# Kernel tuning notes

Hardware: AMD Instinct MI355X
Metric: run time of the kernel (lower is better)

Reference implementation:

```python
import jax, jax.numpy as jnp
import numpy as np

B, S, D = 1, 4096, 1024
H, DH = 8, 128
SCALING = 256.0 ** -0.5
SOFTCAP = 50.0
WINDOW = 512
EPS = 1e-6
NEG = -1e30


def setup_inputs() -> dict:
    key = jax.random.key(0)
    ks = jax.random.split(key, 8)
    hidden_states = jax.random.normal(ks[0], (B, S, D), dtype=jnp.float32)
    # rope tables: plausible cos/sin in [-1,1]
    inv_freq = 1.0 / (10000.0 ** (jnp.arange(0, DH, 2, dtype=jnp.float32) / DH))
    t = jnp.arange(S, dtype=jnp.float32)
    freqs = jnp.outer(t, inv_freq)  # [S, DH/2]
    emb = jnp.concatenate([freqs, freqs], axis=-1)  # [S, DH]
    cos = jnp.cos(emb)[None]  # [1, S, DH]
    sin = jnp.sin(emb)[None]
    w = 0.02
    Wq = jax.random.normal(ks[1], (H * DH, D), dtype=jnp.float32) * w
    Wk = jax.random.normal(ks[2], (H * DH, D), dtype=jnp.float32) * w
    Wv = jax.random.normal(ks[3], (H * DH, D), dtype=jnp.float32) * w
    Wo = jax.random.normal(ks[4], (D, H * DH), dtype=jnp.float32) * w
    q_norm_w = jnp.zeros((DH,), dtype=jnp.float32)
    k_norm_w = jnp.zeros((DH,), dtype=jnp.float32)
    return {"hidden_states": hidden_states, "cos": cos, "sin": sin,
            "Wq": Wq, "Wk": Wk, "Wv": Wv, "Wo": Wo,
            "q_norm_w": q_norm_w, "k_norm_w": k_norm_w}


def _rms_norm(x, w):
    # Gemma3 RMSNorm: x * rsqrt(mean(x^2) + eps) * (1 + w)
    var = jnp.mean(jnp.square(x), axis=-1, keepdims=True)
    return x * jax.lax.rsqrt(var + EPS) * (1.0 + w)


def _rotate_half(x):
    x1, x2 = jnp.split(x, 2, axis=-1)
    return jnp.concatenate([-x2, x1], axis=-1)


def reference(hidden_states, cos, sin, Wq, Wk, Wv, Wo, q_norm_w, k_norm_w):
    b, s, _ = hidden_states.shape
    # QKV projections -> [B, H, S, DH]
    q = (hidden_states @ Wq.T).reshape(b, s, H, DH).transpose(0, 2, 1, 3)
    k = (hidden_states @ Wk.T).reshape(b, s, H, DH).transpose(0, 2, 1, 3)
    v = (hidden_states @ Wv.T).reshape(b, s, H, DH).transpose(0, 2, 1, 3)
    # per-head RMSNorm on q and k
    q = _rms_norm(q, q_norm_w)
    k = _rms_norm(k, k_norm_w)
    # RoPE (cos/sin broadcast over heads via unsqueeze(1))
    c = cos[:, None, :, :]
    si = sin[:, None, :, :]
    q = q * c + _rotate_half(q) * si
    k = k * c + _rotate_half(k) * si
    # scores with scaling and logit softcapping
    scores = jnp.einsum('bhqd,bhkd->bhqk', q, k) * SCALING
    scores = SOFTCAP * jnp.tanh(scores / SOFTCAP)
    # causal + sliding-window mask: attend to j with 0 <= i - j < WINDOW (plus j == i)
    i = jnp.arange(s)[:, None]
    j = jnp.arange(s)[None, :]
    mask = (j <= i) & (i - j < WINDOW)  # [S, S]
    scores = jnp.where(mask[None, None], scores, NEG)
    probs = jax.nn.softmax(scores, axis=-1)  # [B, H, S, S]
    attn = jnp.einsum('bhqk,bhkd->bhqd', probs, v)
    attn = attn.transpose(0, 2, 1, 3).reshape(b, s, H * DH)
    out = attn @ Wo.T
    return out, probs
```

## Files before the change

### kernel.cpp

```cpp
#include <hip/hip_runtime.h>

#define S_LEN 4096

typedef _Float16 f16;
typedef __bf16 bf16;
typedef __attribute__((ext_vector_type(4))) _Float16 f16x4;
typedef __attribute__((ext_vector_type(8))) _Float16 f16x8;
typedef __attribute__((ext_vector_type(8))) __bf16 bf16x8;
typedef __attribute__((ext_vector_type(4))) float f32x4;

__device__ __forceinline__ void async_cp16(void* lds, const void* g) {
  __builtin_amdgcn_global_load_lds((const __attribute__((address_space(1))) void*)g,
                                   (__attribute__((address_space(3))) void*)lds, 16, 0, 0);
}

__device__ __forceinline__ f32x4 mfma16(f16x8 a, f16x8 b, f32x4 c) {
  return __builtin_amdgcn_mfma_f32_16x16x32_f16(a, b, c, 0, 0, 0);
}

__global__ void detect_dtype(const unsigned short* __restrict__ x, int* __restrict__ flag) {
  const int t = threadIdx.x;
  int cnt = 0;
  for (int i = t; i < 16384; i += 256) {
    const int e = (x[i] >> 7) & 0xFF;
    cnt += (e >= 0x87);
  }
#pragma unroll
  for (int m = 1; m < 64; m <<= 1) cnt += __shfl_xor(cnt, m);
  __shared__ int red[4];
  if ((t & 63) == 0) red[t >> 6] = cnt;
  __syncthreads();
  if (t == 0) *flag = (red[0] + red[1] + red[2] + red[3] > 64) ? 1 : 0;
}

__device__ __forceinline__ void cvt8(const void* src, f16* dst, int i, int fp) {
  f16x8 o;
  if (fp) {
    const float* s = (const float*)src;
#pragma unroll
    for (int j = 0; j < 8; ++j) o[j] = (f16)s[i + j];
  } else {
    const bf16x8 v = *(const bf16x8*)((const bf16*)src + i);
#pragma unroll
    for (int j = 0; j < 8; ++j) o[j] = (f16)(float)v[j];
  }
  *(f16x8*)(dst + i) = o;
}

__global__ void cvt_all(const void* __restrict__ hs, const void* __restrict__ wq,
                        const void* __restrict__ wk, const void* __restrict__ wv,
                        const void* __restrict__ wo, const void* __restrict__ c,
                        const void* __restrict__ s, const void* __restrict__ qn,
                        const void* __restrict__ kn, f16* __restrict__ hsf,
                        f16* __restrict__ wqkv, f16* __restrict__ woh,
                        float* __restrict__ cd, float* __restrict__ sd,
                        float* __restrict__ qnd, float* __restrict__ knd,
                        const int* __restrict__ flagp) {
  const int fp = *flagp;
  const int b = blockIdx.x, tid = threadIdx.x;
  if (b < 2048) {
    cvt8(hs, hsf, (b * 256 + tid) * 8, fp);
  } else if (b < 4096) {
    const int bb = b - 2048;
    const int sub = bb >> 9;
    const int i = ((bb & 511) * 256 + tid) * 8;
    const void* src = (sub == 0) ? wq : (sub == 1) ? wk : (sub == 2) ? wv : wo;
    f16* dst = (sub < 3) ? (wqkv + (size_t)sub * 1048576) : woh;
    cvt8(src, dst, i, fp);
  } else if (b < 8192) {
    const int bb = b - 4096;
    const void* src = (bb < 2048) ? c : s;
    float* dst = (bb < 2048) ? cd : sd;
    const int i = (bb & 2047) * 256 + tid;
    dst[i] = fp ? ((const float*)src)[i] : (float)((const bf16*)src)[i];
  } else {
    if (tid < 128) qnd[tid] = fp ? ((const float*)qn)[tid] : (float)((const bf16*)qn)[tid];
    else knd[tid - 128] = fp ? ((const float*)kn)[tid - 128] : (float)((const bf16*)kn)[tid - 128];
  }
}

__launch_bounds__(256, 2)
__global__ void gemm_qkv(const f16* __restrict__ A, const f16* __restrict__ B,
                         const float* __restrict__ cosp, const float* __restrict__ sinp,
                         const float* __restrict__ qnw, const float* __restrict__ knw,
                         f16* __restrict__ qh, f16* __restrict__ kh, f16* __restrict__ vt) {
  __shared__ f16 smem[16384];
  f16* As = smem;
  f16* Bs = smem + 8192;
  const int tid = threadIdx.x;
  const int w = tid >> 6, l = tid & 63;
  const int n0 = blockIdx.x * 128, m0 = blockIdx.y * 128;
  const int wm = (w >> 1) * 64, wn = (w & 1) * 64;
  f32x4 acc[4][4] = {};
  for (int k0 = 0; k0 < 1024; k0 += 64) {
#pragma unroll
    for (int it = 0; it < 4; ++it) {
      const int c = it * 4 + w;
      const int row = c * 8 + (l >> 3);
      const int dq = (l & 7) ^ (row & 7);
      async_cp16(&As[c * 512], &A[(size_t)(m0 + row) * 1024 + k0 + dq * 8]);
      async_cp16(&Bs[c * 512], &B[(size_t)(n0 + row) * 1024 + k0 + dq * 8]);
    }
    __syncthreads();
#pragma unroll
    for (int ks = 0; ks < 2; ++ks) {
      f16x8 af[4], bfr[4];
#pragma unroll
      for (int i = 0; i < 4; ++i) {
        const int ra = wm + i * 16 + (l & 15);
        af[i] = *(const f16x8*)&As[ra * 64 + (((ks * 4 + (l >> 4)) ^ (ra & 7)) << 3)];
        const int rb = wn + i * 16 + (l & 15);
        bfr[i] = *(const f16x8*)&Bs[rb * 64 + (((ks * 4 + (l >> 4)) ^ (rb & 7)) << 3)];
      }
#pragma unroll
      for (int mi = 0; mi < 4; ++mi)
#pragma unroll
        for (int ni = 0; ni < 4; ++ni)
          acc[mi][ni] = mfma16(af[mi], bfr[ni], acc[mi][ni]);
    }
    __syncthreads();
  }
  const int part = blockIdx.x >> 3;
  const int h = blockIdx.x & 7;
#pragma unroll
  for (int mi = 0; mi < 4; ++mi)
#pragma unroll
    for (int ni = 0; ni < 4; ++ni) {
      const int col = wn + ni * 16 + (l & 15);
#pragma unroll
      for (int r = 0; r < 4; ++r) {
        const int row = wm + mi * 16 + ((l >> 4) << 2) + r;
        smem[row * 128 + (col ^ (((row >> 3) & 7) << 3))] = (f16)acc[mi][ni][r];
      }
    }
  __syncthreads();
  if (part == 2) {
#pragma unroll
    for (int it = 0; it < 8; ++it) {
      const int idx = it * 256 + tid;
      const int dh = idx >> 4;
      const int sl = (idx & 15) * 8;
      f16x8 o;
#pragma unroll
      for (int k = 0; k < 8; ++k)
        o[k] = smem[(sl + k) * 128 + (dh ^ ((((sl + k) >> 3) & 7) << 3))];
      *(f16x8*)&vt[((size_t)(h * 128 + dh)) * S_LEN + m0 + sl] = o;
    }
  } else {
    const float* nw = part ? knw : qnw;
    f16* outb = part ? kh : qh;
    const float nw0 = 1.f + nw[l], nw1 = 1.f + nw[l + 64];
#pragma unroll 4
    for (int rr = 0; rr < 32; ++rr) {
      const int row = w * 32 + rr;
      const int sg = m0 + row;
      const int cs = ((row >> 3) & 7) << 3;
      const float x0 = (float)smem[row * 128 + (l ^ cs)];
      const float x1 = (float)smem[row * 128 + ((l + 64) ^ cs)];
      float ssum = x0 * x0 + x1 * x1;
#pragma unroll
      for (int m = 1; m < 64; m <<= 1) ssum += __shfl_xor(ssum, m);
      const float rn = rsqrtf(ssum * (1.f / 128.f) + 1e-6f);
      const float g0 = rn * nw0, g1 = rn * nw1;
      const float c0 = cosp[sg * 128 + l], c1 = cosp[sg * 128 + l + 64];
      const float s0 = sinp[sg * 128 + l], s1 = sinp[sg * 128 + l + 64];
      f16* o = outb + ((size_t)h * S_LEN + sg) * 128;
      o[l] = (f16)(x0 * g0 * c0 - x1 * g1 * s0);
      o[l + 64] = (f16)(x1 * g1 * c1 + x0 * g0 * s1);
    }
  }
}

__launch_bounds__(256, 2)
__global__ void attn64(const f16* __restrict__ Qh, const f16* __restrict__ Kh,
                       const f16* __restrict__ Vt, f16* __restrict__ Pc,
                       float* __restrict__ Lsg, f16* __restrict__ Oh) {
  __shared__ f16 Qs[64 * 128];
  __shared__ f16 Ks[2 * 64 * 128];
  __shared__ f16 Vs[2 * 128 * 64];
  const int tid = threadIdx.x, w = tid >> 6, l = tid & 63;
  const int q0 = blockIdx.x * 64, h = blockIdx.y;
  const int kt0 = (q0 >= 512) ? ((q0 - 511) >> 6) : 0;
  const int kt1 = (q0 + 64) >> 6;

#pragma unroll
  for (int it = 0; it < 4; ++it) {
    const int c = it * 4 + w;
    const int row = c * 4 + (l >> 4);
    const int dq = (l & 15) ^ (row & 15);
    async_cp16(&Qs[c * 512], &Qh[((size_t)h * S_LEN + q0 + row) * 128 + dq * 8]);
  }
#pragma unroll
  for (int it = 0; it < 4; ++it) {
    const int c = it * 4 + w;
    { const int row = c * 4 + (l >> 4);
      const int dq = (l & 15) ^ (row & 15);
      async_cp16(&Ks[c * 512], &Kh[((size_t)h * S_LEN + kt0 * 64 + row) * 128 + dq * 8]); }
    { const int row = c * 8 + (l >> 3);
      const int dq = (l & 7) ^ (row & 7);
      async_cp16(&Vs[c * 512], &Vt[((size_t)h * 128 + row) * S_LEN + kt0 * 64 + dq * 8]); }
  }
  __syncthreads();
  f16x8 qfrag[4];
#pragma unroll
  for (int ks = 0; ks < 4; ++ks) {
    const int r = w * 16 + (l & 15);
    qfrag[ks] = *(const f16x8*)&Qs[r * 128 + (((ks * 4 + (l >> 4)) ^ (r & 15)) << 3)];
  }
  __syncthreads();

  f16* Ps = Qs + w * 1024;
  float l_i[4] = {0.f, 0.f, 0.f, 0.f};
  f32x4 oacc[8] = {};

  for (int t = kt0; t < kt1; ++t) {
    const int cur = (t - kt0) & 1;
    const int kb = cur * 8192, vb = cur * 8192;
    if (t + 1 < kt1) {
      const int nb = (cur ^ 1) * 8192;
#pragma unroll
      for (int it = 0; it < 4; ++it) {
        const int c = it * 4 + w;
        { const int row = c * 4 + (l >> 4);
          const int dq = (l & 15) ^ (row & 15);
          async_cp16(&Ks[nb + c * 512],
                     &Kh[((size_t)h * S_LEN + (t + 1) * 64 + row) * 128 + dq * 8]); }
        { const int row = c * 8 + (l >> 3);
          const int dq = (l & 7) ^ (row & 7);
          async_cp16(&Vs[nb + c * 512],
                     &Vt[((size_t)h * 128 + row) * S_LEN + (t + 1) * 64 + dq * 8]); }
      }
    }
    f32x4 sacc[4] = {};
    __builtin_amdgcn_s_setprio(1);
#pragma unroll
    for (int ks = 0; ks < 4; ++ks) {
      f16x8 kfrag[4];
#pragma unroll
      for (int ni = 0; ni < 4; ++ni) {
        const int r = ni * 16 + (l & 15);
        kfrag[ni] = *(const f16x8*)&Ks[kb + r * 128 + (((ks * 4 + (l >> 4)) ^ (r & 15)) << 3)];
      }
#pragma unroll
      for (int ni = 0; ni < 4; ++ni)
        sacc[ni] = mfma16(qfrag[ks], kfrag[ni], sacc[ni]);
    }
    __builtin_amdgcn_s_setprio(0);
#pragma unroll
    for (int reg = 0; reg < 4; ++reg) {
      const int pr = ((l >> 4) << 2) + reg;
      const int q = q0 + w * 16 + pr;
      float rs = 0.f;
#pragma unroll
      for (int ni = 0; ni < 4; ++ni) {
        const int col = t * 64 + ni * 16 + (l & 15);
        float s = sacc[ni][reg] * 0.0625f;
        const float z = __expf(s * 0.04f);
        s = 50.f * (1.f - 2.f / (z + 1.f));
        const bool valid = (col <= q) && (q - col < 512);
        const float p = valid ? __expf(s - 8.f) : 0.f;
        rs += p;
        const int pc = ni * 16 + (l & 15);
        Ps[pr * 64 + (((pc >> 3) ^ (pr & 7)) << 3) + (pc & 7)] = (f16)p;
      }
#pragma unroll
      for (int m = 1; m < 16; m <<= 1) rs += __shfl_xor(rs, m);
      l_i[reg] += rs;
    }
    __builtin_amdgcn_s_setprio(1);
#pragma unroll
    for (int ks = 0; ks < 2; ++ks) {
      const int rp = l & 15;
      const f16x8 pf = *(const f16x8*)&Ps[rp * 64 + (((ks * 4 + (l >> 4)) ^ (rp & 7)) << 3)];
      f16x8 vf[8];
#pragma unroll
      for (int ni = 0; ni < 8; ++ni) {
        const int r = ni * 16 + (l & 15);
        vf[ni] = *(const f16x8*)&Vs[vb + r * 64 + (((ks * 4 + (l >> 4)) ^ (r & 7)) << 3)];
      }
#pragma unroll
      for (int ni = 0; ni < 8; ++ni)
        oacc[ni] = mfma16(pf, vf[ni], oacc[ni]);
    }
    __builtin_amdgcn_s_setprio(0);
    {
      const size_t rowbase = (size_t)h * 4096 + q0 + w * 16;
#pragma unroll
      for (int i = 0; i < 4; ++i) {
        const int pr = i * 4 + (l >> 4);
        const int pc = (l & 15) * 4;
        const f16x4 v = *(const f16x4*)&Ps[pr * 64 + (((pc >> 3) ^ (pr & 7)) << 3) + (pc & 7)];
        *(f16x4*)&Pc[(rowbase + pr) * 576 + (t - kt0) * 64 + pc] = v;
      }
    }
    __syncthreads();
  }

  float il[4];
#pragma unroll
  for (int r = 0; r < 4; ++r) il[r] = 1.f / l_i[r];
  if ((l & 15) == 0) {
#pragma unroll
    for (int r = 0; r < 4; ++r)
      Lsg[(h << 12) + q0 + w * 16 + ((l >> 4) << 2) + r] = il[r];
  }
#pragma unroll
  for (int ni = 0; ni < 8; ++ni) {
    const int row = q0 + w * 16 + ((l >> 4) << 2);
    const int col = h * 128 + ni * 16 + (l & 15);
#pragma unroll
    for (int r = 0; r < 4; ++r)
      Oh[(size_t)(row + r) * 1024 + col] = (f16)(oacc[ni][r] * il[r]);
  }
}

__launch_bounds__(256, 2)
__global__ void gemmO_probs(const f16* __restrict__ A, const f16* __restrict__ B,
                            void* __restrict__ dout, const f16* __restrict__ Pc,
                            const float* __restrict__ Lsg, const int* __restrict__ flagp) {
  __shared__ f16 smem[16384];
  const int fp = *flagp;
  const int tid = threadIdx.x;
  if (blockIdx.x < 256) {
    f16* As = smem;
    f16* Bs = smem + 8192;
    const int w = tid >> 6, l = tid & 63;
    const int n0 = (blockIdx.x & 7) * 128, m0 = (blockIdx.x >> 3) * 128;
    const int wm = (w >> 1) * 64, wn = (w & 1) * 64;
    f32x4 acc[4][4] = {};
    for (int k0 = 0; k0 < 1024; k0 += 64) {
#pragma unroll
      for (int it = 0; it < 4; ++it) {
        const int c = it * 4 + w;
        const int row = c * 8 + (l >> 3);
        const int dq = (l & 7) ^ (row & 7);
        async_cp16(&As[c * 512], &A[(size_t)(m0 + row) * 1024 + k0 + dq * 8]);
        async_cp16(&Bs[c * 512], &B[(size_t)(n0 + row) * 1024 + k0 + dq * 8]);
      }
      __syncthreads();
#pragma unroll
      for (int ks = 0; ks < 2; ++ks) {
        f16x8 af[4], bfr[4];
#pragma unroll
        for (int i = 0; i < 4; ++i) {
          const int ra = wm + i * 16 + (l & 15);
          af[i] = *(const f16x8*)&As[ra * 64 + (((ks * 4 + (l >> 4)) ^ (ra & 7)) << 3)];
          const int rb = wn + i * 16 + (l & 15);
          bfr[i] = *(const f16x8*)&Bs[rb * 64 + (((ks * 4 + (l >> 4)) ^ (rb & 7)) << 3)];
        }
#pragma unroll
        for (int mi = 0; mi < 4; ++mi)
#pragma unroll
          for (int ni = 0; ni < 4; ++ni)
            acc[mi][ni] = mfma16(af[mi], bfr[ni], acc[mi][ni]);
      }
      __syncthreads();
    }
#pragma unroll
    for (int mi = 0; mi < 4; ++mi)
#pragma unroll
      for (int ni = 0; ni < 4; ++ni) {
        const int col = n0 + wn + ni * 16 + (l & 15);
        const int row = m0 + wm + mi * 16 + ((l >> 4) << 2);
#pragma unroll
        for (int r = 0; r < 4; ++r) {
          const size_t off = (size_t)(row + r) * 1024 + col;
          if (fp) ((float*)dout)[off] = acc[mi][ni][r];
          else    ((bf16*)dout)[off] = (bf16)acc[mi][ni][r];
        }
      }
  } else {
    const long long stride = (long long)(gridDim.x - 256) * 256;
    const long long base = (long long)(blockIdx.x - 256) * 256 + tid;
    if (fp) {
      float* pb = (float*)dout + 4194304;
      const long long total = 8LL * 4096 * 1024;
      auto do4 = [&](long long idx) {
        const int h = (int)(idx >> 22);
        const int rem = (int)(idx & 4194303);
        const int row = rem >> 10;
        const int c = (rem & 1023) << 2;
        const int q0r = row & ~63;
        const int jc0 = (q0r >= 512) ? (((q0r - 511) >> 6) << 6) : 0;
        f32x4 v = {};
        if (c >= jc0 && c < q0r + 64) {
          const float sc = Lsg[(h << 12) + row];
          const f16x4 pv = *(const f16x4*)&Pc[((size_t)(h << 12) + row) * 576 + (c - jc0)];
#pragma unroll
          for (int k = 0; k < 4; ++k) v[k] = (float)pv[k] * sc;
        }
        __builtin_nontemporal_store(v, (f32x4*)&pb[((size_t)h << 24) + ((size_t)row << 12) + c]);
      };
      for (long long i0 = base; i0 < total; i0 += 2 * stride) {
        do4(i0);
        if (i0 + stride < total) do4(i0 + stride);
      }
    } else {
      bf16* pb = (bf16*)dout + 4194304;
      const long long total = 8LL * 4096 * 512;
      auto do8 = [&](long long idx) {
        const int h = (int)(idx >> 21);
        const int rem = (int)(idx & 2097151);
        const int row = rem >> 9;
        const int c = (rem & 511) << 3;
        const int q0r = row & ~63;
        const int jc0 = (q0r >= 512) ? (((q0r - 511) >> 6) << 6) : 0;
        bf16x8 v = {};
        if (c >= jc0 && c < q0r + 64) {
          const float sc = Lsg[(h << 12) + row];
          const f16x8 pv = *(const f16x8*)&Pc[((size_t)(h << 12) + row) * 576 + (c - jc0)];
#pragma unroll
          for (int k = 0; k < 8; ++k) v[k] = (bf16)((float)pv[k] * sc);
        }
        __builtin_nontemporal_store(v, (bf16x8*)&pb[((size_t)h << 24) + ((size_t)row << 12) + c]);
      };
      for (long long i0 = base; i0 < total; i0 += 2 * stride) {
        do8(i0);
        if (i0 + stride < total) do8(i0 + stride);
      }
    }
  }
}

extern "C" void kernel_launch(void* const* d_in, const int* in_sizes, int n_in,
                              void* d_out, int out_size, void* d_ws, size_t ws_size,
                              hipStream_t stream) {
  (void)in_sizes; (void)n_in; (void)out_size; (void)ws_size;
  char* ws = (char*)d_ws;
  f16*   Pc    = (f16*)(ws);
  f16*   qh    = (f16*)(ws + (36u << 20));
  f16*   kh    = (f16*)(ws + (44u << 20));
  f16*   vt    = (f16*)(ws + (52u << 20));
  f16*   attnh = (f16*)(ws + (60u << 20));
  f16*   woh   = (f16*)(ws + (68u << 20));
  f16*   hsf   = (f16*)(ws + (70u << 20));
  float* Lsg   = (float*)(ws + (70u << 20));
  f16*   wqkv  = (f16*)(ws + (78u << 20));
  float* cosf  = (float*)(ws + (84u << 20));
  float* sinf  = (float*)(ws + (86u << 20));
  float* qnwf  = (float*)(ws + (88u << 20));
  float* knwf  = (float*)(ws + (88u << 20) + 512);
  int*   flag  = (int*)(ws + (88u << 20) + 1024);

  detect_dtype<<<1, 256, 0, stream>>>((const unsigned short*)d_in[0], flag);
  cvt_all<<<8193, 256, 0, stream>>>(d_in[0], d_in[3], d_in[4], d_in[5], d_in[6],
                                    d_in[1], d_in[2], d_in[7], d_in[8],
                                    hsf, wqkv, woh, cosf, sinf, qnwf, knwf, flag);
  gemm_qkv<<<dim3(24, 32), 256, 0, stream>>>(hsf, wqkv, cosf, sinf, qnwf, knwf, qh, kh, vt);
  attn64<<<dim3(64, 8), 256, 0, stream>>>(qh, kh, vt, Pc, Lsg, attnh);
  gemmO_probs<<<2048, 256, 0, stream>>>(attnh, woh, d_out, Pc, Lsg, flag);
}
```

Before: 670.1 us.

## Move probs zero-fill into QKV GEMM launch and write only the band later

After: 676.7 us. No clear change (+1.0%).

```diff
diff --git a/kernel.cpp b/kernel.cpp
--- a/kernel.cpp
+++ b/kernel.cpp
@@ -79,17 +79,56 @@
   }
 }
 
+__device__ __forceinline__ void probs_zero_fill(void* dout, int fp, int fb, int nfb) {
+  const int tid = threadIdx.x;
+  if (fp) {
+    float* pb = (float*)dout + 4194304;
+    const int total = 8 * 4096 * 880;
+    const f32x4 z = {};
+    for (int u = fb * 256 + tid; u < total; u += nfb * 256) {
+      const int rowid = (int)((unsigned)u / 880u);
+      const int cu = u - rowid * 880;
+      const int row = rowid & 4095;
+      const int q0r = row & ~63;
+      const int jc0 = (q0r >= 512) ? (((q0r - 511) >> 6) << 6) : 0;
+      const int jc0c = jc0 >> 2;
+      const int c4 = (cu < jc0c) ? (cu << 2) : (jc0 + 576 + ((cu - jc0c) << 2));
+      __builtin_nontemporal_store(z, (f32x4*)&pb[((size_t)rowid << 12) + c4]);
+    }
+  } else {
+    bf16* pb = (bf16*)dout + 4194304;
+    const int total = 8 * 4096 * 440;
+    const bf16x8 z = {};
+    for (int u = fb * 256 + tid; u < total; u += nfb * 256) {
+      const int rowid = (int)((unsigned)u / 440u);
+      const int cu = u - rowid * 440;
+      const int row = rowid & 4095;
+      const int q0r = row & ~63;
+      const int jc0 = (q0r >= 512) ? (((q0r - 511) >> 6) << 6) : 0;
+      const int jc0c = jc0 >> 3;
+      const int c8 = (cu < jc0c) ? (cu << 3) : (jc0 + 576 + ((cu - jc0c) << 3));
+      __builtin_nontemporal_store(z, (bf16x8*)&pb[((size_t)rowid << 12) + c8]);
+    }
+  }
+}
+
 __launch_bounds__(256, 2)
 __global__ void gemm_qkv(const f16* __restrict__ A, const f16* __restrict__ B,
                          const float* __restrict__ cosp, const float* __restrict__ sinp,
                          const float* __restrict__ qnw, const float* __restrict__ knw,
-                         f16* __restrict__ qh, f16* __restrict__ kh, f16* __restrict__ vt) {
+                         f16* __restrict__ qh, f16* __restrict__ kh, f16* __restrict__ vt,
+                         void* __restrict__ dout, const int* __restrict__ flagp) {
   __shared__ f16 smem[16384];
+  const int id = blockIdx.x;
+  if (id >= 768) {
+    probs_zero_fill(dout, *flagp, id - 768, gridDim.x - 768);
+    return;
+  }
   f16* As = smem;
   f16* Bs = smem + 8192;
   const int tid = threadIdx.x;
   const int w = tid >> 6, l = tid & 63;
-  const int n0 = blockIdx.x * 128, m0 = blockIdx.y * 128;
+  const int n0 = (id % 24) * 128, m0 = (id / 24) * 128;
   const int wm = (w >> 1) * 64, wn = (w & 1) * 64;
   f32x4 acc[4][4] = {};
   for (int k0 = 0; k0 < 1024; k0 += 64) {
@@ -120,8 +159,8 @@
     }
     __syncthreads();
   }
-  const int part = blockIdx.x >> 3;
-  const int h = blockIdx.x & 7;
+  const int part = (id % 24) >> 3;
+  const int h = id & 7;
 #pragma unroll
   for (int mi = 0; mi < 4; ++mi)
 #pragma unroll
@@ -370,53 +409,44 @@
         }
       }
   } else {
-    const long long stride = (long long)(gridDim.x - 256) * 256;
-    const long long base = (long long)(blockIdx.x - 256) * 256 + tid;
+    const int bb = blockIdx.x - 256, nbb = gridDim.x - 256;
     if (fp) {
       float* pb = (float*)dout + 4194304;
-      const long long total = 8LL * 4096 * 1024;
-      auto do4 = [&](long long idx) {
-        const int h = (int)(idx >> 22);
-        const int rem = (int)(idx & 4194303);
-        const int row = rem >> 10;
-        const int c = (rem & 1023) << 2;
+      const int total = 8 * 4096 * 144;
+      for (int u = bb * 256 + tid; u < total; u += nbb * 256) {
+        const int rowid = (int)((unsigned)u / 144u);
+        const int cu = u - rowid * 144;
+        const int row = rowid & 4095;
         const int q0r = row & ~63;
         const int jc0 = (q0r >= 512) ? (((q0r - 511) >> 6) << 6) : 0;
+        const int c4 = jc0 + (cu << 2);
         f32x4 v = {};
-        if (c >= jc0 && c < q0r + 64) {
-          const float sc = Lsg[(h << 12) + row];
-          const f16x4 pv = *(const f16x4*)&Pc[((size_t)(h << 12) + row) * 576 + (c - jc0)];
+        if (c4 < q0r + 64) {
+          const float sc = Lsg[rowid];
+          const f16x4 pv = *(const f16x4*)&Pc[(size_t)rowid * 576 + (cu << 2)];
 #pragma unroll
           for (int k = 0; k < 4; ++k) v[k] = (float)pv[k] * sc;
         }
-        __builtin_nontemporal_store(v, (f32x4*)&pb[((size_t)h << 24) + ((size_t)row << 12) + c]);
-      };
-      for (long long i0 = base; i0 < total; i0 += 2 * stride) {
-        do4(i0);
-        if (i0 + stride < total) do4(i0 + stride);
+        __builtin_nontemporal_store(v, (f32x4*)&pb[((size_t)rowid << 12) + c4]);
       }
     } else {
       bf16* pb = (bf16*)dout + 4194304;
-      const long long total = 8LL * 4096 * 512;
-      auto do8 = [&](long long idx) {
-        const int h = (int)(idx >> 21);
-        const int rem = (int)(idx & 2097151);
-        const int row = rem >> 9;
-        const int c = (rem & 511) << 3;
+      const int total = 8 * 4096 * 72;
+      for (int u = bb * 256 + tid; u < total; u += nbb * 256) {
+        const int rowid = (int)((unsigned)u / 72u);
+        const int cu = u - rowid * 72;
+        const int row = rowid & 4095;
         const int q0r = row & ~63;
         const int jc0 = (q0r >= 512) ? (((q0r - 511) >> 6) << 6) : 0;
+        const int c8 = jc0 + (cu << 3);
         bf16x8 v = {};
-        if (c >= jc0 && c < q0r + 64) {
-          const float sc = Lsg[(h << 12) + row];
-          const f16x8 pv = *(const f16x8*)&Pc[((size_t)(h << 12) + row) * 576 + (c - jc0)];
+        if (c8 < q0r + 64) {
+          const float sc = Lsg[rowid];
+          const f16x8 pv = *(const f16x8*)&Pc[(size_t)rowid * 576 + (cu << 3)];
 #pragma unroll
           for (int k = 0; k < 8; ++k) v[k] = (bf16)((float)pv[k] * sc);
         }
-        __builtin_nontemporal_store(v, (bf16x8*)&pb[((size_t)h << 24) + ((size_t)row << 12) + c]);
-      };
-      for (long long i0 = base; i0 < total; i0 += 2 * stride) {
-        do8(i0);
-        if (i0 + stride < total) do8(i0 + stride);
+        __builtin_nontemporal_store(v, (bf16x8*)&pb[((size_t)rowid << 12) + c8]);
       }
     }
   }
@@ -446,7 +476,8 @@
   cvt_all<<<8193, 256, 0, stream>>>(d_in[0], d_in[3], d_in[4], d_in[5], d_in[6],
                                     d_in[1], d_in[2], d_in[7], d_in[8],
                                     hsf, wqkv, woh, cosf, sinf, qnwf, knwf, flag);
-  gemm_qkv<<<dim3(24, 32), 256, 0, stream>>>(hsf, wqkv, cosf, sinf, qnwf, knwf, qh, kh, vt);
+  gemm_qkv<<<2048, 256, 0, stream>>>(hsf, wqkv, cosf, sinf, qnwf, knwf, qh, kh, vt,
+                                     d_out, flag);
   attn64<<<dim3(64, 8), 256, 0, stream>>>(qh, kh, vt, Pc, Lsg, attnh);
-  gemmO_probs<<<2048, 256, 0, stream>>>(attnh, woh, d_out, Pc, Lsg, flag);
-}
+  gemmO_probs<<<768, 256, 0, stream>>>(attnh, woh, d_out, Pc, Lsg, flag);
+}
```
